# Kernel tuning notes

Hardware: AMD Instinct MI355X
Metric: run time of the kernel (lower is better)

The kernel has to match this reference:

```python
import jax, jax.numpy as jnp
import numpy as np

EPS = 1e-6


def _ring_view(t, start, length, M):
    # contiguous logical view of `length` oldest positions starting at start
    if start + length <= M:
        return t[:, start:start + length]
    first = t[:, start:]
    return jnp.concatenate([first, t[:, :length - first.shape[1]]], axis=1)


def _ring_write(t, start, chunk, M):
    # write chunk at logical position `start`, wrapping around the ring
    C = chunk.shape[1]
    if start + C <= M:
        return t.at[:, start:start + C].set(chunk)
    first = M - start
    t = t.at[:, start:].set(chunk[:, :first])
    return t.at[:, :C - first].set(chunk[:, first:])


def setup_inputs() -> dict:
    key = jax.random.key(0)
    ks = jax.random.split(key, 9)
    B, M, Hh, D, F, C = 4, 1088, 32, 128, 128, 512
    f = lambda k, s: jax.random.normal(k, s, dtype=jnp.float32)
    return {
        "K": f(ks[0], (B, M, Hh, D)),
        "V": f(ks[1], (B, M, Hh, D)),
        "FK": f(ks[2], (B, M, Hh, F)),
        "H": f(ks[3], (B, Hh, F, D)),
        "S": f(ks[4], (B, Hh, F)),
        "k_c": f(ks[5], (B, C, Hh, D)),
        "v_c": f(ks[6], (B, C, Hh, D)),
        "fk_c": f(ks[7], (B, C, Hh, F)),
        "fq": f(ks[8], (B, C, Hh, F)),
        "write_ptr": 100,
        "valid": 1088,
    }


def reference(K, V, FK, H, S, k_c, v_c, fk_c, fq, write_ptr, valid):
    M = K.shape[1]
    C = k_c.shape[1]
    if valid + C <= M:
        # room left in ring buffer: plain write, no eviction
        pos = (write_ptr + valid) % M
        K = _ring_write(K, pos, k_c, M)
        V = _ring_write(V, pos, v_c, M)
        FK = _ring_write(FK, pos, fk_c, M)
    else:
        # evict num_excess oldest tokens into recurrent state H, S
        num_excess = valid + C - M
        old_fk = _ring_view(FK, write_ptr, num_excess, M)  # (B, E, H, F)
        old_v = _ring_view(V, write_ptr, num_excess, M)    # (B, E, H, D)
        H = H + jnp.einsum('behf,behd->bhfd', old_fk, old_v)
        S = S + old_fk.sum(axis=1)
        write_ptr = (write_ptr + num_excess) % M
        pos = (write_ptr + M) % M  # valid == M now
        K = _ring_write(K, pos, k_c, M)
        V = _ring_write(V, pos, v_c, M)
        FK = _ring_write(FK, pos, fk_c, M)
    # linear_attn_forward(fq)
    y_num = jnp.einsum('bchf,bhfd->bchd', fq, H)
    y_den = jnp.einsum('bchf,bhf->bch', fq, S)[..., None]
    return y_num, y_den, K, V, FK, H, S
```

## Files before the change

kernel.cpp:

```cpp
#include <hip/hip_runtime.h>

typedef float f32x4 __attribute__((ext_vector_type(4)));

constexpr int B  = 4;
constexpr int M  = 1088;
constexpr int HH = 32;
constexpr int D  = 128;
constexpr int F  = 128;
constexpr int C  = 512;

constexpr int SZ_YNUM = B * C * HH * D;
constexpr int SZ_YDEN = B * C * HH;
constexpr int SZ_KVM  = B * M * HH * D;
constexpr int SZ_H    = B * HH * F * D;

constexpr int OFF_YNUM = 0;
constexpr int OFF_YDEN = OFF_YNUM + SZ_YNUM;
constexpr int OFF_K    = OFF_YDEN + SZ_YDEN;
constexpr int OFF_V    = OFF_K + SZ_KVM;
constexpr int OFF_FK   = OFF_V + SZ_KVM;
constexpr int OFF_H    = OFF_FK + SZ_KVM;
constexpr int OFF_S    = OFF_H + SZ_H;

constexpr int INNER4      = HH * D / 4;
constexpr int ROWS_PER_CB = 4;
constexpr int COPY_BLOCKS = B * M / ROWS_PER_CB;
constexpr int HS_BLOCKS   = B * HH * 2;
constexpr int Y_BLOCKS    = B * HH * 8;

__device__ __forceinline__ void ring_params(const int* wp_p, const int* valid_p,
                                            int& wp, int& num_excess, int& pos) {
    wp = *wp_p;
    int valid = *valid_p;
    if (valid + C <= M) {
        num_excess = 0;
        pos = (wp + valid) % M;
    } else {
        num_excess = valid + C - M;
        pos = (wp + num_excess) % M;
    }
}

__device__ __forceinline__ void ring_copy_block(int cb, int tid,
                                                const f32x4* __restrict__ src,
                                                const f32x4* __restrict__ chk,
                                                f32x4* __restrict__ dst,
                                                int pos) {
    int bm0 = cb * ROWS_PER_CB;
#pragma unroll
    for (int r = 0; r < ROWS_PER_CB; ++r) {
        int bm = bm0 + r;
        int m = bm % M;
        int b = bm / M;
        int off = m - pos;
        if (off < 0) off += M;
        const f32x4* s = (off < C) ? &chk[(b * C + off) * INNER4]
                                   : &src[bm * INNER4];
        f32x4* d = &dst[bm * INNER4];
#pragma unroll
        for (int k = 0; k < INNER4 / 256; ++k)
            d[k * 256 + tid] = s[k * 256 + tid];
    }
}

constexpr int ESTEP = 32;

__device__ void update_hs_body(int bx,
                               const float* __restrict__ FKi,
                               const float* __restrict__ Vi,
                               const float* __restrict__ Hi,
                               const float* __restrict__ Si,
                               float* __restrict__ Ho,
                               float* __restrict__ So,
                               int wp, int num_excess) {
    const int tid = threadIdx.x;
    const int fhalf = bx & 1;
    const int bh = bx >> 1;
    const int h = bh & (HH - 1);
    const int b = bh >> 5;
    const int fbase = fhalf * 64;

    __shared__ float  fk_s[2][ESTEP][64];
    __shared__ f32x4  v_s[2][ESTEP][32];
    __shared__ float  sred[4][64];

    const int tf = tid >> 5;
    const int td = tid & 31;
    const int cq = tid & 63;
    const int qq = tid >> 6;

    f32x4 acc[8];
#pragma unroll
    for (int i = 0; i < 8; ++i) acc[i] = (f32x4)0.f;
    float s_part = 0.f;

    float fkA[8], fkB[8];
    f32x4 vA[4],  vB[4];

    auto load_tile = [&](int e0, float* fk_r, f32x4* v_r) {
#pragma unroll
        for (int j = 0; j < 8; ++j) {
            int e = e0 + qq + 4 * j;
            int me = wp + e;
            if (me >= M) me -= M;
            if (me >= M) me -= M;
            float v = 0.f;
            if (e < num_excess) v = FKi[((b * M + me) * HH + h) * F + fbase + cq];
            fk_r[j] = v;
        }
#pragma unroll
        for (int j = 0; j < 4; ++j) {
            int e = e0 + tf + 8 * j;
            int me = wp + e;
            if (me >= M) me -= M;
            if (me >= M) me -= M;
            f32x4 v = (f32x4)0.f;
            if (e < num_excess) v = *(const f32x4*)&Vi[((b * M + me) * HH + h) * D + td * 4];
            v_r[j] = v;
        }
    };
    auto store_tile = [&](const float* fk_r, const f32x4* v_r, int buf) {
#pragma unroll
        for (int j = 0; j < 8; ++j) fk_s[buf][qq + 4 * j][cq] = fk_r[j];
#pragma unroll
        for (int j = 0; j < 4; ++j) v_s[buf][tf + 8 * j][td] = v_r[j];
    };
    auto compute = [&](int buf) {
#pragma unroll
        for (int ee = 0; ee < ESTEP; ++ee) {
            f32x4 fa = *(const f32x4*)&fk_s[buf][ee][tf * 8];
            f32x4 fb = *(const f32x4*)&fk_s[buf][ee][tf * 8 + 4];
            f32x4 vv = v_s[buf][ee][td];
            acc[0] += fa.x * vv; acc[1] += fa.y * vv;
            acc[2] += fa.z * vv; acc[3] += fa.w * vv;
            acc[4] += fb.x * vv; acc[5] += fb.y * vv;
            acc[6] += fb.z * vv; acc[7] += fb.w * vv;
        }
#pragma unroll
        for (int j = 0; j < 8; ++j) s_part += fk_s[buf][qq * 8 + j][cq];
    };

    if (num_excess > 0) {
        const int nt = (num_excess + ESTEP - 1) / ESTEP;
        load_tile(0, fkA, vA);
        if (nt > 1) load_tile(ESTEP, fkB, vB);
        store_tile(fkA, vA, 0);
        for (int t = 0; t < nt; t += 2) {
            __syncthreads();
            if (t + 1 < nt) store_tile(fkB, vB, 1);
            if (t + 2 < nt) load_tile((t + 2) * ESTEP, fkA, vA);
            compute(0);
            if (t + 1 >= nt) break;
            __syncthreads();
            if (t + 2 < nt) store_tile(fkA, vA, 0);
            if (t + 3 < nt) load_tile((t + 3) * ESTEP, fkB, vB);
            compute(1);
        }
    }

    sred[qq][cq] = s_part;
    __syncthreads();
    if (tid < 64) {
        int f = fbase + tid;
        int si = (b * HH + h) * F + f;
        So[si] = Si[si] + sred[0][tid] + sred[1][tid] + sred[2][tid] + sred[3][tid];
    }

#pragma unroll
    for (int i = 0; i < 8; ++i) {
        int f = fbase + tf * 8 + i;
        int base = ((b * HH + h) * F + f) * D + td * 4;
        f32x4 hold = *(const f32x4*)&Hi[base];
        *(f32x4*)&Ho[base] = hold + acc[i];
    }
}

__device__ void compute_y_den_body(int bx,
                                   const float* __restrict__ fq,
                                   const float* __restrict__ Hn,
                                   const float* __restrict__ Sn,
                                   float* __restrict__ ynum,
                                   float* __restrict__ yden) {
    const int tid = threadIdx.x;
    int t0 = bx;
    const int ct = t0 & 7; t0 >>= 3;
    const int h = t0 & (HH - 1);
    const int b = t0 >> 5;
    const int c0 = ct * 64;

    __shared__ float  fq_s[32][65];
    __shared__ f32x4  h_s[32][32];
    __shared__ float  S_s[128];
    __shared__ float  den_s[64][4];

    const int tc = tid >> 5;
    const int td = tid & 31;
    const int cq = tid & 63;
    const int qq = tid >> 6;

    if (tid < 128) S_s[tid] = Sn[(b * HH + h) * F + tid];

    f32x4 acc[8];
#pragma unroll
    for (int i = 0; i < 8; ++i) acc[i] = (f32x4)0.f;
    float den_part = 0.f;

    float fqr[8];
    f32x4 hr[4];
    const int lcc = tid >> 5, lee = tid & 31;
    const int lrow = tid >> 6, lcol = tid & 63;

    auto load_step = [&](int f0) {
#pragma unroll
        for (int r = 0; r < 8; ++r) {
            int cc = lcc + r * 8;
            fqr[r] = fq[((b * C + c0 + cc) * HH + h) * F + f0 + lee];
        }
#pragma unroll
        for (int r = 0; r < 4; ++r) {
            int idx = tid + r * 256;
            int row = idx >> 5, col = idx & 31;
            hr[r] = *(const f32x4*)&Hn[((b * HH + h) * F + f0 + row) * D + col * 4];
        }
    };
    auto store_step = [&]() {
#pragma unroll
        for (int r = 0; r < 8; ++r) fq_s[lee][lcc + r * 8] = fqr[r];
#pragma unroll
        for (int r = 0; r < 4; ++r) {
            int idx = tid + r * 256;
            int row = idx >> 5, col = idx & 31;
            h_s[row][col] = hr[r];
        }
    };

    load_step(0);
    store_step();
    for (int step = 0; step < 4; ++step) {
        bool more = step + 1 < 4;
        if (more) load_step((step + 1) * 32);
        __syncthreads();
#pragma unroll
        for (int ee = 0; ee < 32; ++ee) {
            f32x4 hv = h_s[ee][td];
#pragma unroll
            for (int i = 0; i < 8; ++i) {
                float q = fq_s[ee][tc * 8 + i];
                acc[i] += q * hv;
            }
        }
#pragma unroll
        for (int j = 0; j < 8; ++j)
            den_part += fq_s[qq * 8 + j][cq] * S_s[step * 32 + qq * 8 + j];
        __syncthreads();
        if (more) store_step();
    }

    den_s[cq][qq] = den_part;
    __syncthreads();
    if (tid < 64)
        yden[(b * C + c0 + tid) * HH + h] =
            den_s[tid][0] + den_s[tid][1] + den_s[tid][2] + den_s[tid][3];

#pragma unroll
    for (int i = 0; i < 8; ++i) {
        int c = c0 + tc * 8 + i;
        int base = ((b * C + c) * HH + h) * D + td * 4;
        *(f32x4*)&ynum[base] = acc[i];
    }
}

__global__ __launch_bounds__(256) void fused_hs_vfk(
        const float* __restrict__ FKi, const float* __restrict__ Vi,
        const float* __restrict__ Hi,  const float* __restrict__ Si,
        float* __restrict__ Ho,        float* __restrict__ So,
        const f32x4* __restrict__ V4,  const f32x4* __restrict__ vc,  f32x4* __restrict__ oV,
        const f32x4* __restrict__ FK4, const f32x4* __restrict__ fkc, f32x4* __restrict__ oFK,
        const int* __restrict__ wp_p,  const int* __restrict__ valid_p) {
    int wp, num_excess, pos;
    ring_params(wp_p, valid_p, wp, num_excess, pos);

    int bx = blockIdx.x;
    if (bx < HS_BLOCKS) {
        update_hs_body(bx, FKi, Vi, Hi, Si, Ho, So, wp, num_excess);
        return;
    }
    bx -= HS_BLOCKS;
    if (bx < COPY_BLOCKS) {
        ring_copy_block(bx, threadIdx.x, V4, vc, oV, pos);
        return;
    }
    bx -= COPY_BLOCKS;
    ring_copy_block(bx, threadIdx.x, FK4, fkc, oFK, pos);
}

__global__ __launch_bounds__(256) void fused_y_k(
        const float* __restrict__ fq, const float* __restrict__ Hn,
        const float* __restrict__ Sn,
        float* __restrict__ ynum,     float* __restrict__ yden,
        const f32x4* __restrict__ K4, const f32x4* __restrict__ kc,
        f32x4* __restrict__ oK,
        const int* __restrict__ wp_p, const int* __restrict__ valid_p) {
    int wp, num_excess, pos;
    ring_params(wp_p, valid_p, wp, num_excess, pos);

    int bx = blockIdx.x;
    if (bx < Y_BLOCKS) {
        compute_y_den_body(bx, fq, Hn, Sn, ynum, yden);
        return;
    }
    bx -= Y_BLOCKS;
    ring_copy_block(bx, threadIdx.x, K4, kc, oK, pos);
}

extern "C" void kernel_launch(void* const* d_in, const int* in_sizes, int n_in,
                              void* d_out, int out_size, void* d_ws, size_t ws_size,
                              hipStream_t stream) {
    const float* K   = (const float*)d_in[0];
    const float* V   = (const float*)d_in[1];
    const float* FK  = (const float*)d_in[2];
    const float* H   = (const float*)d_in[3];
    const float* S   = (const float*)d_in[4];
    const float* k_c = (const float*)d_in[5];
    const float* v_c = (const float*)d_in[6];
    const float* fk_c= (const float*)d_in[7];
    const float* fq  = (const float*)d_in[8];
    const int* wp    = (const int*)d_in[9];
    const int* valid = (const int*)d_in[10];

    float* out = (float*)d_out;
    float* o_ynum = out + OFF_YNUM;
    float* o_yden = out + OFF_YDEN;
    float* o_K    = out + OFF_K;
    float* o_V    = out + OFF_V;
    float* o_FK   = out + OFF_FK;
    float* o_H    = out + OFF_H;
    float* o_S    = out + OFF_S;

    fused_hs_vfk<<<HS_BLOCKS + 2 * COPY_BLOCKS, 256, 0, stream>>>(
        FK, V, H, S, o_H, o_S,
        (const f32x4*)V,  (const f32x4*)v_c,  (f32x4*)o_V,
        (const f32x4*)FK, (const f32x4*)fk_c, (f32x4*)o_FK,
        wp, valid);

    fused_y_k<<<Y_BLOCKS + COPY_BLOCKS, 256, 0, stream>>>(
        fq, o_H, o_S, o_ynum, o_yden,
        (const f32x4*)K, (const f32x4*)k_c, (f32x4*)o_K,
        wp, valid);
}
```

Baseline: 158.8 us.

## Shrink HS tiles to single LDS buffer and drop Y register prefetch

The H/S update now uses a single shared-memory tile of 16 evicted rows instead of double-buffered 32-row tiles, with smaller register staging arrays and an extra barrier per tile. The y_num/y_den stage drops its register prefetch pipeline and loads fq and H straight into shared memory each step. Both changes cut LDS and register footprint, which may raise occupancy. The cost is less overlap between global loads and compute and more barriers.

New measurement: 152.6 us. 1.04x faster.

```diff
diff --git a/kernel.cpp b/kernel.cpp
--- a/kernel.cpp
+++ b/kernel.cpp
@@ -27,6 +27,7 @@
 constexpr int COPY_BLOCKS = B * M / ROWS_PER_CB;
 constexpr int HS_BLOCKS   = B * HH * 2;
 constexpr int Y_BLOCKS    = B * HH * 8;
+constexpr int ESTEP       = 16;
 
 __device__ __forceinline__ void ring_params(const int* wp_p, const int* valid_p,
                                             int& wp, int& num_excess, int& pos) {
@@ -62,8 +63,6 @@
             d[k * 256 + tid] = s[k * 256 + tid];
     }
 }
-
-constexpr int ESTEP = 32;
 
 __device__ void update_hs_body(int bx,
                                const float* __restrict__ FKi,
@@ -80,8 +79,8 @@
     const int b = bh >> 5;
     const int fbase = fhalf * 64;
 
-    __shared__ float  fk_s[2][ESTEP][64];
-    __shared__ f32x4  v_s[2][ESTEP][32];
+    __shared__ float  fk_s[ESTEP][64];
+    __shared__ f32x4  v_s[ESTEP][32];
     __shared__ float  sred[4][64];
 
     const int tf = tid >> 5;
@@ -94,12 +93,12 @@
     for (int i = 0; i < 8; ++i) acc[i] = (f32x4)0.f;
     float s_part = 0.f;
 
-    float fkA[8], fkB[8];
-    f32x4 vA[4],  vB[4];
+    float fkA[4], fkB[4];
+    f32x4 vA[2],  vB[2];
 
     auto load_tile = [&](int e0, float* fk_r, f32x4* v_r) {
 #pragma unroll
-        for (int j = 0; j < 8; ++j) {
+        for (int j = 0; j < 4; ++j) {
             int e = e0 + qq + 4 * j;
             int me = wp + e;
             if (me >= M) me -= M;
@@ -109,7 +108,7 @@
             fk_r[j] = v;
         }
 #pragma unroll
-        for (int j = 0; j < 4; ++j) {
+        for (int j = 0; j < 2; ++j) {
             int e = e0 + tf + 8 * j;
             int me = wp + e;
             if (me >= M) me -= M;
@@ -119,42 +118,45 @@
             v_r[j] = v;
         }
     };
-    auto store_tile = [&](const float* fk_r, const f32x4* v_r, int buf) {
-#pragma unroll
-        for (int j = 0; j < 8; ++j) fk_s[buf][qq + 4 * j][cq] = fk_r[j];
-#pragma unroll
-        for (int j = 0; j < 4; ++j) v_s[buf][tf + 8 * j][td] = v_r[j];
+    auto store_tile = [&](const float* fk_r, const f32x4* v_r) {
+#pragma unroll
+        for (int j = 0; j < 4; ++j) fk_s[qq + 4 * j][cq] = fk_r[j];
+#pragma unroll
+        for (int j = 0; j < 2; ++j) v_s[tf + 8 * j][td] = v_r[j];
     };
-    auto compute = [&](int buf) {
+    auto compute = [&]() {
 #pragma unroll
         for (int ee = 0; ee < ESTEP; ++ee) {
-            f32x4 fa = *(const f32x4*)&fk_s[buf][ee][tf * 8];
-            f32x4 fb = *(const f32x4*)&fk_s[buf][ee][tf * 8 + 4];
-            f32x4 vv = v_s[buf][ee][td];
+            f32x4 fa = *(const f32x4*)&fk_s[ee][tf * 8];
+            f32x4 fb = *(const f32x4*)&fk_s[ee][tf * 8 + 4];
+            f32x4 vv = v_s[ee][td];
             acc[0] += fa.x * vv; acc[1] += fa.y * vv;
             acc[2] += fa.z * vv; acc[3] += fa.w * vv;
             acc[4] += fb.x * vv; acc[5] += fb.y * vv;
             acc[6] += fb.z * vv; acc[7] += fb.w * vv;
         }
 #pragma unroll
-        for (int j = 0; j < 8; ++j) s_part += fk_s[buf][qq * 8 + j][cq];
+        for (int j = 0; j < 4; ++j) s_part += fk_s[qq * 4 + j][cq];
     };
 
     if (num_excess > 0) {
         const int nt = (num_excess + ESTEP - 1) / ESTEP;
         load_tile(0, fkA, vA);
         if (nt > 1) load_tile(ESTEP, fkB, vB);
-        store_tile(fkA, vA, 0);
+        store_tile(fkA, vA);
         for (int t = 0; t < nt; t += 2) {
             __syncthreads();
-            if (t + 1 < nt) store_tile(fkB, vB, 1);
             if (t + 2 < nt) load_tile((t + 2) * ESTEP, fkA, vA);
-            compute(0);
+            compute();
+            __syncthreads();
             if (t + 1 >= nt) break;
+            store_tile(fkB, vB);
             __syncthreads();
-            if (t + 2 < nt) store_tile(fkA, vA, 0);
             if (t + 3 < nt) load_tile((t + 3) * ESTEP, fkB, vB);
-            compute(1);
+            compute();
+            __syncthreads();
+            if (t + 2 >= nt) break;
+            store_tile(fkA, vA);
         }
     }
 
@@ -187,6 +189,7 @@
     const int h = t0 & (HH - 1);
     const int b = t0 >> 5;
     const int c0 = ct * 64;
+    const int bh = b * HH + h;
 
     __shared__ float  fq_s[32][65];
     __shared__ f32x4  h_s[32][32];
@@ -198,47 +201,26 @@
     const int cq = tid & 63;
     const int qq = tid >> 6;
 
-    if (tid < 128) S_s[tid] = Sn[(b * HH + h) * F + tid];
+    if (tid < 128) S_s[tid] = Sn[bh * F + tid];
 
     f32x4 acc[8];
 #pragma unroll
     for (int i = 0; i < 8; ++i) acc[i] = (f32x4)0.f;
     float den_part = 0.f;
 
-    float fqr[8];
-    f32x4 hr[4];
-    const int lcc = tid >> 5, lee = tid & 31;
-    const int lrow = tid >> 6, lcol = tid & 63;
-
-    auto load_step = [&](int f0) {
+    for (int f0 = 0; f0 < F; f0 += 32) {
 #pragma unroll
         for (int r = 0; r < 8; ++r) {
-            int cc = lcc + r * 8;
-            fqr[r] = fq[((b * C + c0 + cc) * HH + h) * F + f0 + lee];
+            int idx = tid + r * 256;
+            int cc = idx >> 5, ee = idx & 31;
+            fq_s[ee][cc] = fq[((b * C + c0 + cc) * HH + h) * F + f0 + ee];
         }
 #pragma unroll
         for (int r = 0; r < 4; ++r) {
             int idx = tid + r * 256;
             int row = idx >> 5, col = idx & 31;
-            hr[r] = *(const f32x4*)&Hn[((b * HH + h) * F + f0 + row) * D + col * 4];
-        }
-    };
-    auto store_step = [&]() {
-#pragma unroll
-        for (int r = 0; r < 8; ++r) fq_s[lee][lcc + r * 8] = fqr[r];
-#pragma unroll
-        for (int r = 0; r < 4; ++r) {
-            int idx = tid + r * 256;
-            int row = idx >> 5, col = idx & 31;
-            h_s[row][col] = hr[r];
-        }
-    };
-
-    load_step(0);
-    store_step();
-    for (int step = 0; step < 4; ++step) {
-        bool more = step + 1 < 4;
-        if (more) load_step((step + 1) * 32);
+            h_s[row][col] = *(const f32x4*)&Hn[(bh * F + f0 + row) * D + col * 4];
+        }
         __syncthreads();
 #pragma unroll
         for (int ee = 0; ee < 32; ++ee) {
@@ -251,9 +233,8 @@
         }
 #pragma unroll
         for (int j = 0; j < 8; ++j)
-            den_part += fq_s[qq * 8 + j][cq] * S_s[step * 32 + qq * 8 + j];
+            den_part += fq_s[qq * 8 + j][cq] * S_s[f0 + qq * 8 + j];
         __syncthreads();
-        if (more) store_step();
     }
 
     den_s[cq][qq] = den_part;
```
